# Kernel optimization log

Measured on AMD Instinct MI355X. Metric: run time of the kernel, lower is better.

Reference implementation:

```python
import jax, jax.numpy as jnp
import numpy as np

# hyper_params (mode='test')
PRE_NMS = 1000
POST_NMS = 300
IOU_TH = 0.7
VARIANCES = np.array([0.1, 0.1, 0.2, 0.2], dtype=np.float32)
FM = 64            # feature map height/width
ANCHOR_COUNT = 9   # 3 scales x 3 ratios


def _make_anchors():
    """Normalized [y1,x1,y2,x2] anchors on a FM x FM grid, 9 per cell."""
    scales = np.array([0.1, 0.2, 0.4], np.float32)
    ratios = np.array([0.5, 1.0, 2.0], np.float32)
    ws = (scales[:, None] * np.sqrt(ratios)[None, :]).reshape(-1)  # (9,)
    hs = (scales[:, None] / np.sqrt(ratios)[None, :]).reshape(-1)  # (9,)
    ctr = (np.arange(FM, dtype=np.float32) + 0.5) / FM
    cy, cx = np.meshgrid(ctr, ctr, indexing='ij')                  # (FM,FM)
    cy = cy[..., None]; cx = cx[..., None]                         # (FM,FM,1)
    anchors = np.stack([cy - 0.5 * hs, cx - 0.5 * ws,
                        cy + 0.5 * hs, cx + 0.5 * ws], axis=-1)    # (FM,FM,9,4)
    return jnp.asarray(anchors.reshape(-1, 4))                     # (36864,4)


def setup_inputs() -> dict:
    key = jax.random.key(0)
    k1, k2 = jax.random.split(key)
    B = 16
    rpn_bbox_deltas = jax.random.normal(k1, (B, FM, FM, ANCHOR_COUNT * 4), dtype=jnp.float32)
    rpn_labels = jax.random.uniform(k2, (B, FM, FM, ANCHOR_COUNT), dtype=jnp.float32)
    return {"rpn_bbox_deltas": rpn_bbox_deltas,
            "rpn_labels": rpn_labels,
            "anchors": _make_anchors()}


def _nms_single(boxes):
    """Greedy NMS on score-sorted boxes (N,4) -> (POST_NMS,4), zero-padded."""
    N = boxes.shape[0]
    y1, x1, y2, x2 = boxes[:, 0], boxes[:, 1], boxes[:, 2], boxes[:, 3]
    area = (y2 - y1) * (x2 - x1)                                   # (N,)
    iy1 = jnp.maximum(y1[:, None], y1[None, :])
    ix1 = jnp.maximum(x1[:, None], x1[None, :])
    iy2 = jnp.minimum(y2[:, None], y2[None, :])
    ix2 = jnp.minimum(x2[:, None], x2[None, :])
    inter = jnp.maximum(iy2 - iy1, 0.0) * jnp.maximum(ix2 - ix1, 0.0)
    iou = inter / jnp.maximum(area[:, None] + area[None, :] - inter, 1e-9)  # (N,N)
    idx = jnp.arange(N)

    def body(i, keep):
        # if box i survives, suppress later boxes with high overlap
        suppress = keep[i] & (iou[i] > IOU_TH) & (idx > i)
        return keep & ~suppress

    keep = jax.lax.fori_loop(0, N, body, jnp.ones((N,), dtype=bool))
    # stable sort: kept boxes first, original (score-descending) order preserved
    order = jnp.argsort(jnp.where(keep, 0, 1))[:POST_NMS]
    sel = boxes[order]
    valid = keep[order]
    # combined_non_max_suppression clips output boxes to [0,1] and zero-pads
    return jnp.where(valid[:, None], jnp.clip(sel, 0.0, 1.0), 0.0)


def reference(rpn_bbox_deltas, rpn_labels, anchors):
    B = rpn_bbox_deltas.shape[0]
    N = anchors.shape[0]
    deltas = rpn_bbox_deltas.reshape(B, N, 4) * jnp.asarray(VARIANCES)
    labels = rpn_labels.reshape(B, N)

    # decode deltas against anchors
    anc_h = anchors[:, 2] - anchors[:, 0]
    anc_w = anchors[:, 3] - anchors[:, 1]
    anc_cy = anchors[:, 0] + 0.5 * anc_h
    anc_cx = anchors[:, 1] + 0.5 * anc_w
    h = jnp.exp(deltas[..., 2]) * anc_h
    w = jnp.exp(deltas[..., 3]) * anc_w
    cy = deltas[..., 0] * anc_h + anc_cy
    cx = deltas[..., 1] * anc_w + anc_cx
    boxes = jnp.stack([cy - 0.5 * h, cx - 0.5 * w,
                       cy + 0.5 * h, cx + 0.5 * w], axis=-1)       # (B,N,4)

    # top-k by objectness score (descending, so NMS input is pre-sorted)
    _, pre_idx = jax.lax.top_k(labels, PRE_NMS)                    # (B,PRE_NMS)
    pre_boxes = jnp.take_along_axis(boxes, pre_idx[..., None], axis=1)  # (B,PRE_NMS,4)

    roi_bboxes = jax.vmap(_nms_single)(pre_boxes)                  # (B,POST_NMS,4)
    return jax.lax.stop_gradient(roi_bboxes)
```

## Files before the change

### kernel.cpp

```cpp
#include <hip/hip_runtime.h>
#include <stdint.h>

#pragma clang fp contract(off)

#define N_ANCH 36864
#define PRE_NMS 1000
#define POST_NMS 300
#define SEL_CAP 1024
#define NWAVE 16

#define SLICES 16
#define K1_NT 256
#define SLICE_KEYS 2304
#define KEYS_PT 9
#define SLICE_TOP 128
#define COMPACT_CAP 192
#define MERGE_CAP 2048

#define NCOPY 8
#define HSTR 257

#define M_WSTRIDE 1024
#define M_WORDS_PER_B 16384
#define WS_BOX_FLOATS_PER_B 5120

__device__ __forceinline__ uint32_t mono_key(float v) {
    uint32_t u = __float_as_uint(v);
    return (u & 0x80000000u) ? ~u : (u | 0x80000000u);
}

__device__ __forceinline__ float clip01(float x) {
    return fminf(fmaxf(x, 0.0f), 1.0f);
}

__device__ __forceinline__ uint64_t bcast64(uint64_t v, int srclane) {
    uint32_t lo = (uint32_t)v, hi = (uint32_t)(v >> 32);
    lo = __builtin_amdgcn_readlane(lo, srclane);
    hi = __builtin_amdgcn_readlane(hi, srclane);
    return ((uint64_t)hi << 32) | (uint64_t)lo;
}

__device__ __forceinline__ uint64_t sfl64(uint64_t v) {
    uint32_t lo = __builtin_amdgcn_readfirstlane((uint32_t)v);
    uint32_t hi = __builtin_amdgcn_readfirstlane((uint32_t)(v >> 32));
    return ((uint64_t)hi << 32) | (uint64_t)lo;
}

__device__ __forceinline__ uint64_t bfly_or64(uint64_t v) {
    v |= __shfl_xor(v, 32);
    v |= __shfl_xor(v, 16);
    v |= __shfl_xor(v, 8);
    v |= __shfl_xor(v, 4);
    v |= __shfl_xor(v, 2);
    v |= __shfl_xor(v, 1);
    return v;
}

__device__ __forceinline__ void scan256(const uint32_t* __restrict__ h, uint32_t K,
                                        uint32_t* shm, uint32_t& outBin, uint32_t& outKrem) {
    const int t    = threadIdx.x;
    const int lane = t & 63;
    const int wv   = t >> 6;
    const uint32_t q = h[t];
    uint32_t sfx = q, o;
    o = __shfl_down(sfx, 1);  if (lane < 63) sfx += o;
    o = __shfl_down(sfx, 2);  if (lane < 62) sfx += o;
    o = __shfl_down(sfx, 4);  if (lane < 60) sfx += o;
    o = __shfl_down(sfx, 8);  if (lane < 56) sfx += o;
    o = __shfl_down(sfx, 16); if (lane < 48) sfx += o;
    o = __shfl_down(sfx, 32); if (lane < 32) sfx += o;
    if (lane == 0) shm[wv] = sfx;
    __syncthreads();
    uint32_t wAbove = 0;
    for (int w2 = wv + 1; w2 < 4; ++w2) wAbove += shm[w2];
    const uint32_t above = wAbove + (sfx - q);
    if ((above < K) && (above + q >= K)) { shm[4] = (uint32_t)t; shm[5] = K - above; }
    __syncthreads();
    outBin  = shm[4];
    outKrem = shm[5];
}

__global__ __launch_bounds__(K1_NT) void k1s_slice_top(
    const float* __restrict__ labels,
    uint64_t* __restrict__ wsCand)
{
    const int s = blockIdx.x;
    const int b = blockIdx.y;
    const int t = threadIdx.x;
    const int lane = t & 63;

    __shared__ uint32_t hc[NCOPY * HSTR];
    __shared__ uint32_t red[256];
    __shared__ uint32_t shm[8];
    __shared__ uint64_t cand[COMPACT_CAP];
    __shared__ uint32_t scnt;

    const float* lab = labels + (size_t)b * N_ANCH + (size_t)s * SLICE_KEYS;
    uint32_t key[KEYS_PT];
#pragma unroll
    for (int r = 0; r < KEYS_PT; ++r)
        key[r] = mono_key(lab[r * K1_NT + t]);

    for (int i = t; i < NCOPY * HSTR; i += K1_NT) hc[i] = 0u;
    if (t == 0) scnt = 0u;
    __syncthreads();

    const int cbase = (lane & 7) * HSTR;
#pragma unroll
    for (int r = 0; r < KEYS_PT; ++r)
        atomicAdd(&hc[cbase + (key[r] >> 24)], 1u);
    __syncthreads();
    uint32_t sum = 0;
#pragma unroll
    for (int c = 0; c < NCOPY; ++c) sum += hc[c * HSTR + t];
    red[t] = sum;
    __syncthreads();
    uint32_t b0, krem;
    scan256(red, SLICE_TOP, shm, b0, krem);
    __syncthreads();

    red[t] = 0u;
    __syncthreads();
#pragma unroll
    for (int r = 0; r < KEYS_PT; ++r)
        if ((key[r] >> 24) == b0) atomicAdd(&red[(key[r] >> 16) & 0xFFu], 1u);
    __syncthreads();
    uint32_t b1, krem2;
    scan256(red, krem, shm, b1, krem2);
    const uint32_t thresh16 = (b0 << 8) | b1;

#pragma unroll
    for (int r = 0; r < KEYS_PT; ++r) {
        const uint32_t u = key[r];
        if ((u >> 16) >= thresh16) {
            const uint32_t gi = (uint32_t)(s * SLICE_KEYS + r * K1_NT + t);
            uint32_t pos = atomicAdd(&scnt, 1u);
            if (pos < COMPACT_CAP)
                cand[pos] = ((uint64_t)u << 32) | (uint64_t)(0xFFFFFFFFu - gi);
        }
    }
    __syncthreads();
    uint32_t c = scnt; if (c > COMPACT_CAP) c = COMPACT_CAP;
    if (t >= (int)c && t < COMPACT_CAP) cand[t] = 0ull;
    __syncthreads();

    if (t < COMPACT_CAP) {
        const uint64_t mine = cand[t];
        uint32_t rank = 0;
        for (int i = 0; i < COMPACT_CAP; i += 4)
            rank += (cand[i]     > mine) + (cand[i + 1] > mine)
                  + (cand[i + 2] > mine) + (cand[i + 3] > mine);
        if (t < (int)c && rank < SLICE_TOP)
            wsCand[((size_t)b * SLICES + s) * SLICE_TOP + rank] = mine;
    }
}

__global__ __launch_bounds__(K1_NT) void k1m_merge_decode(
    const float* __restrict__ deltas,
    const float* __restrict__ anchors,
    const uint64_t* __restrict__ wsCand,
    float* __restrict__ wsBox)
{
    const int chunk = blockIdx.x;
    const int b     = blockIdx.y;
    const int t     = threadIdx.x;

    __shared__ uint64_t keyA[MERGE_CAP];
    const uint64_t* c2 = wsCand + (size_t)b * MERGE_CAP;
    for (int i = t; i < MERGE_CAP; i += K1_NT) keyA[i] = c2[i];
    __syncthreads();

    if (t < SLICE_TOP) {
        const uint64_t mine = keyA[chunk * SLICE_TOP + t];
        uint32_t rank = 0;
#pragma unroll
        for (int r = 0; r < SLICES; ++r) {
            const uint64_t* a = &keyA[r * SLICE_TOP];
            uint32_t lo = 0;
#pragma unroll
            for (uint32_t s2 = 128; s2 > 0; s2 >>= 1)
                if (lo + s2 <= 128u && a[lo + s2 - 1] > mine) lo += s2;
            rank += lo;
        }
        if (rank < PRE_NMS) {
            uint32_t idx = 0xFFFFFFFFu - (uint32_t)(mine & 0xFFFFFFFFull);
            float4 d4 = *(const float4*)(deltas + ((size_t)b * N_ANCH + idx) * 4);
            float4 a4 = *(const float4*)(anchors + (size_t)idx * 4);
            float anc_h  = a4.z - a4.x;
            float anc_w  = a4.w - a4.y;
            float anc_cy = a4.x + 0.5f * anc_h;
            float anc_cx = a4.y + 0.5f * anc_w;
            float dy = d4.x * 0.1f, dx = d4.y * 0.1f;
            float dh = d4.z * 0.2f, dw = d4.w * 0.2f;
            float h  = expf(dh) * anc_h;
            float w  = expf(dw) * anc_w;
            float cy = dy * anc_h + anc_cy;
            float cx = dx * anc_w + anc_cx;
            float y1 = cy - 0.5f * h, x1 = cx - 0.5f * w;
            float y2 = cy + 0.5f * h, x2 = cx + 0.5f * w;
            float* wb = wsBox + (size_t)b * WS_BOX_FLOATS_PER_B;
            wb[rank]              = y1;
            wb[SEL_CAP + rank]    = x1;
            wb[2*SEL_CAP + rank]  = y2;
            wb[3*SEL_CAP + rank]  = x2;
            wb[4*SEL_CAP + rank]  = (y2 - y1) * (x2 - x1);
        }
    }
}

__global__ __launch_bounds__(1024) void k2_iou_matrix(
    const float* __restrict__ wsBox,
    uint64_t* __restrict__ wsM)
{
    const int gx   = blockIdx.x;
    const int b    = blockIdx.y;
    const int t    = threadIdx.x;
    const int lane = t & 63;
    const int wave = t >> 6;

    int cb, r0, r1;
    if (gx < 16) { cb = gx;     r0 = 0;   r1 = 64 * (cb + 1); if (r1 > 512) r1 = 512; }
    else         { cb = gx - 8; r0 = 512; r1 = 64 * (cb + 1); }
    if (r1 > PRE_NMS) r1 = PRE_NMS;

    __shared__ float s[5 * SEL_CAP];
    const float4* b4 = (const float4*)(wsBox + (size_t)b * WS_BOX_FLOATS_PER_B);
    float4* s4 = (float4*)s;
    for (int i = t; i < (5 * SEL_CAP) / 4; i += 1024) s4[i] = b4[i];
    __syncthreads();

    float* ly1 = s;
    float* lx1 = s + SEL_CAP;
    float* ly2 = s + 2 * SEL_CAP;
    float* lx2 = s + 3 * SEL_CAP;
    float* lar = s + 4 * SEL_CAP;

    const int j = cb * 64 + lane;
    const float y1j = ly1[j], x1j = lx1[j], y2j = ly2[j], x2j = lx2[j], aj = lar[j];

    uint64_t* Mb = wsM + (size_t)b * M_WORDS_PER_B + (size_t)cb * M_WSTRIDE;
    for (int i = r0 + wave; i < r1; i += NWAVE) {
        float iy1 = fmaxf(ly1[i], y1j);
        float ix1 = fmaxf(lx1[i], x1j);
        float iy2 = fminf(ly2[i], y2j);
        float ix2 = fminf(lx2[i], x2j);
        float ih = iy2 - iy1; if (ih < 0.f) ih = 0.f;
        float iw = ix2 - ix1; if (iw < 0.f) iw = 0.f;
        float inter = ih * iw;
        float denom = lar[i] + aj - inter;
        if (denom < 1e-9f) denom = 1e-9f;
        float iou = inter / denom;
        bool sup = (j > i) && (iou > 0.7f);
        uint64_t mask = __ballot(sup ? 1 : 0);
        if (lane == 0) Mb[i] = mask;
    }
}

__global__ __launch_bounds__(1024) void k3_reduce_out(
    const float* __restrict__ wsBox,
    const uint64_t* __restrict__ wsM,
    float* __restrict__ out)
{
    const int b    = blockIdx.x;
    const int t    = threadIdx.x;
    const int lane = t & 63;
    const int wave = t >> 6;

    __shared__ uint64_t remv[16];
    __shared__ uint64_t keepW[16];
    __shared__ uint32_t wordPref[16];

    const uint64_t* Mg = wsM + (size_t)b * M_WORDS_PER_B;

    if (t < 16) remv[t] = 0ull;

    uint64_t mDiag = 0ull, mSup = 0ull, selfC = 0ull;
    if (wave == 0) {
        mDiag = Mg[lane];
        mSup  = Mg[(size_t)1 * M_WSTRIDE + lane];
    }
    __syncthreads();

    for (int w = 0; w < 16; ++w) {
        if (wave == 0) {
            const uint64_t m  = mDiag;
            const uint64_t ms = mSup;
            if (w < 15) {
                mDiag = Mg[(size_t)(w + 1) * M_WSTRIDE + 64 * (w + 1) + lane];
                if (w < 14)
                    mSup = Mg[(size_t)(w + 2) * M_WSTRIDE + 64 * (w + 1) + lane];
            }
            const uint64_t valid = (w == 15) ? ((1ull << 40) - 1ull) : ~0ull;
            const bool laneValid = (w < 15) || (lane < 40);

            const uint64_t amS = sfl64(bfly_or64(laneValid ? m : 0ull));

            uint64_t cur = sfl64(remv[w] | selfC);

            const uint64_t Q        = amS & ~cur & valid;
            const uint64_t keptSure = valid & ~cur & ~Q;

            cur |= sfl64(bfly_or64(((keptSure >> lane) & 1ull) ? m : 0ull));

            uint64_t work = Q & ~cur;
            while (work) {
                const int bp = (int)__builtin_ctzll(work);
                cur |= bcast64(m, bp);
                work &= ~(1ull << bp);
                work &= ~cur;
            }

            const uint64_t keep = (~cur) & valid;
            if (lane == 0) keepW[w] = keep;
            if (w < 15)
                selfC = bfly_or64(((keep >> lane) & 1ull) ? ms : 0ull);
        } else if (w >= 1 && wave > w) {
            const uint64_t km = keepW[w - 1];
            uint64_t v = Mg[(size_t)wave * M_WSTRIDE + 64 * (w - 1) + lane];
            v = ((km >> lane) & 1ull) ? v : 0ull;
            v = bfly_or64(v);
            if (lane == 0) remv[wave] |= v;
        }
        __syncthreads();
    }

    if (t == 0) {
        uint32_t acc = 0u;
        for (int w = 0; w < 16; ++w) {
            wordPref[w] = acc;
            acc += (uint32_t)__popcll(keepW[w]);
        }
    }
    float* ob = out + (size_t)b * (POST_NMS * 4);
    for (int i = t; i < POST_NMS * 4; i += 1024) ob[i] = 0.0f;
    __syncthreads();

    if (t < PRE_NMS) {
        const int w = t >> 6, bpos = t & 63;
        uint64_t kw = keepW[w];
        if ((kw >> bpos) & 1ull) {
            uint32_t rank = wordPref[w] +
                            (uint32_t)__popcll(kw & ((1ull << bpos) - 1ull));
            if (rank < POST_NMS) {
                const float* wb = wsBox + (size_t)b * WS_BOX_FLOATS_PER_B;
                float* o = ob + (size_t)rank * 4;
                o[0] = clip01(wb[t]);
                o[1] = clip01(wb[SEL_CAP + t]);
                o[2] = clip01(wb[2*SEL_CAP + t]);
                o[3] = clip01(wb[3*SEL_CAP + t]);
            }
        }
    }
}

extern "C" void kernel_launch(void* const* d_in, const int* in_sizes, int n_in,
                              void* d_out, int out_size, void* d_ws, size_t ws_size,
                              hipStream_t stream) {
    const float* deltas  = (const float*)d_in[0];
    const float* labels  = (const float*)d_in[1];
    const float* anchors = (const float*)d_in[2];
    float* out = (float*)d_out;
    const int B = in_sizes[1] / N_ANCH;

    char* p = (char*)d_ws;
    uint64_t* wsCand = (uint64_t*)p;
    float*    wsBox  = (float*)(p + (size_t)B * MERGE_CAP * 8);
    uint64_t* wsM    = (uint64_t*)(p + (size_t)B * MERGE_CAP * 8
                                     + (size_t)B * WS_BOX_FLOATS_PER_B * 4);

    k1s_slice_top<<<dim3(SLICES, B), K1_NT, 0, stream>>>(labels, wsCand);
    k1m_merge_decode<<<dim3(SLICES, B), K1_NT, 0, stream>>>(deltas, anchors, wsCand, wsBox);
    k2_iou_matrix<<<dim3(24, B), 1024, 0, stream>>>(wsBox, wsM);
    k3_reduce_out<<<B, 1024, 0, stream>>>(wsBox, wsM, out);
}
```

Measured before the change: 110.8 us.

## Fuse IoU matrix and NMS reduce via last-block-done atomic counter

Merges the IoU bitmask kernel and the per-batch greedy reduction kernel into one launch. Each block increments a per-batch atomic counter after writing its mask words, and the last block to finish runs the NMS reduction and output write, reusing the boxes already held in shared memory. This removes one kernel launch and its gap, and the re-read of box data from global memory. In exchange it adds fences and an atomic per block, and the reduction is serialized onto whichever block arrives last.

```diff
diff --git a/kernel.cpp b/kernel.cpp
--- a/kernel.cpp
+++ b/kernel.cpp
@@ -23,6 +23,7 @@
 #define M_WSTRIDE 1024
 #define M_WORDS_PER_B 16384
 #define WS_BOX_FLOATS_PER_B 5120
+#define K2_BLOCKS_PER_B 24
 
 __device__ __forceinline__ uint32_t mono_key(float v) {
     uint32_t u = __float_as_uint(v);
@@ -82,12 +83,15 @@
 
 __global__ __launch_bounds__(K1_NT) void k1s_slice_top(
     const float* __restrict__ labels,
-    uint64_t* __restrict__ wsCand)
+    uint64_t* __restrict__ wsCand,
+    uint32_t* __restrict__ wsCnt)
 {
     const int s = blockIdx.x;
     const int b = blockIdx.y;
     const int t = threadIdx.x;
     const int lane = t & 63;
+
+    if (s == 0 && t == 0) wsCnt[b] = 0u;
 
     __shared__ uint32_t hc[NCOPY * HSTR];
     __shared__ uint32_t red[256];
@@ -208,9 +212,11 @@
     }
 }
 
-__global__ __launch_bounds__(1024) void k2_iou_matrix(
+__global__ __launch_bounds__(1024) void k2b_iou_nms(
     const float* __restrict__ wsBox,
-    uint64_t* __restrict__ wsM)
+    uint64_t* __restrict__ wsM,
+    uint32_t* __restrict__ wsCnt,
+    float* __restrict__ out)
 {
     const int gx   = blockIdx.x;
     const int b    = blockIdx.y;
@@ -254,17 +260,19 @@
         uint64_t mask = __ballot(sup ? 1 : 0);
         if (lane == 0) Mb[i] = mask;
     }
-}
-
-__global__ __launch_bounds__(1024) void k3_reduce_out(
-    const float* __restrict__ wsBox,
-    const uint64_t* __restrict__ wsM,
-    float* __restrict__ out)
-{
-    const int b    = blockIdx.x;
-    const int t    = threadIdx.x;
-    const int lane = t & 63;
-    const int wave = t >> 6;
+    __syncthreads();
+
+    __shared__ uint32_t isWinner;
+    if (t == 0) {
+        __threadfence();
+        uint32_t old = __hip_atomic_fetch_add(&wsCnt[b], 1u,
+                                              __ATOMIC_ACQ_REL,
+                                              __HIP_MEMORY_SCOPE_AGENT);
+        isWinner = (old == (uint32_t)(K2_BLOCKS_PER_B - 1));
+    }
+    __syncthreads();
+    if (!isWinner) return;
+    __threadfence();
 
     __shared__ uint64_t remv[16];
     __shared__ uint64_t keepW[16];
@@ -342,12 +350,11 @@
             uint32_t rank = wordPref[w] +
                             (uint32_t)__popcll(kw & ((1ull << bpos) - 1ull));
             if (rank < POST_NMS) {
-                const float* wb = wsBox + (size_t)b * WS_BOX_FLOATS_PER_B;
                 float* o = ob + (size_t)rank * 4;
-                o[0] = clip01(wb[t]);
-                o[1] = clip01(wb[SEL_CAP + t]);
-                o[2] = clip01(wb[2*SEL_CAP + t]);
-                o[3] = clip01(wb[3*SEL_CAP + t]);
+                o[0] = clip01(ly1[t]);
+                o[1] = clip01(lx1[t]);
+                o[2] = clip01(ly2[t]);
+                o[3] = clip01(lx2[t]);
             }
         }
     }
@@ -367,9 +374,11 @@
     float*    wsBox  = (float*)(p + (size_t)B * MERGE_CAP * 8);
     uint64_t* wsM    = (uint64_t*)(p + (size_t)B * MERGE_CAP * 8
                                      + (size_t)B * WS_BOX_FLOATS_PER_B * 4);
-
-    k1s_slice_top<<<dim3(SLICES, B), K1_NT, 0, stream>>>(labels, wsCand);
+    uint32_t* wsCnt  = (uint32_t*)(p + (size_t)B * MERGE_CAP * 8
+                                     + (size_t)B * WS_BOX_FLOATS_PER_B * 4
+                                     + (size_t)B * M_WORDS_PER_B * 8);
+
+    k1s_slice_top<<<dim3(SLICES, B), K1_NT, 0, stream>>>(labels, wsCand, wsCnt);
     k1m_merge_decode<<<dim3(SLICES, B), K1_NT, 0, stream>>>(deltas, anchors, wsCand, wsBox);
-    k2_iou_matrix<<<dim3(24, B), 1024, 0, stream>>>(wsBox, wsM);
-    k3_reduce_out<<<B, 1024, 0, stream>>>(wsBox, wsM, out);
-}
+    k2b_iou_nms<<<dim3(K2_BLOCKS_PER_B, B), 1024, 0, stream>>>(wsBox, wsM, wsCnt, out);
+}
```

New measurement: 142.9 us. 1.29x slower.

## Fuse merge-rank/decode into IoU kernel and prefetch reduce-stage mask words

Applied to the files above, without the earlier changes.

Drops the separate merge/decode kernel. Each of the 24 IoU blocks per image now ranks all 2048 candidates, decodes the top 1000 boxes straight into shared memory, and builds its IoU tile, so one launch and the global round-trip of the box workspace go away. Block 0 still writes box coordinates to global for the output stage, but no longer writes the area. The merge ranking and decode work is now repeated in every block, which adds redundant compute and extra anchor and delta gathers. The reduce kernel also prefetches the next mask word for the non-leader waves to hide global load latency.

```diff
diff --git a/kernel.cpp b/kernel.cpp
--- a/kernel.cpp
+++ b/kernel.cpp
@@ -155,23 +155,36 @@
     }
 }
 
-__global__ __launch_bounds__(K1_NT) void k1m_merge_decode(
+__global__ __launch_bounds__(1024) void k2f_rank_iou(
     const float* __restrict__ deltas,
     const float* __restrict__ anchors,
     const uint64_t* __restrict__ wsCand,
-    float* __restrict__ wsBox)
+    float* __restrict__ wsBox,
+    uint64_t* __restrict__ wsM)
 {
-    const int chunk = blockIdx.x;
-    const int b     = blockIdx.y;
-    const int t     = threadIdx.x;
+    const int gx   = blockIdx.x;
+    const int b    = blockIdx.y;
+    const int t    = threadIdx.x;
+    const int lane = t & 63;
+    const int wave = t >> 6;
 
     __shared__ uint64_t keyA[MERGE_CAP];
+    __shared__ float s[5 * SEL_CAP];
+
     const uint64_t* c2 = wsCand + (size_t)b * MERGE_CAP;
-    for (int i = t; i < MERGE_CAP; i += K1_NT) keyA[i] = c2[i];
-    __syncthreads();
-
-    if (t < SLICE_TOP) {
-        const uint64_t mine = keyA[chunk * SLICE_TOP + t];
+    for (int i = t; i < MERGE_CAP; i += 1024) keyA[i] = c2[i];
+    __syncthreads();
+
+    float* ly1 = s;
+    float* lx1 = s + SEL_CAP;
+    float* ly2 = s + 2 * SEL_CAP;
+    float* lx2 = s + 3 * SEL_CAP;
+    float* lar = s + 4 * SEL_CAP;
+
+#pragma unroll
+    for (int kk = 0; kk < 2; ++kk) {
+        const int ki = t + kk * 1024;
+        const uint64_t mine = keyA[ki];
         uint32_t rank = 0;
 #pragma unroll
         for (int r = 0; r < SLICES; ++r) {
@@ -198,42 +211,26 @@
             float cx = dx * anc_w + anc_cx;
             float y1 = cy - 0.5f * h, x1 = cx - 0.5f * w;
             float y2 = cy + 0.5f * h, x2 = cx + 0.5f * w;
-            float* wb = wsBox + (size_t)b * WS_BOX_FLOATS_PER_B;
-            wb[rank]              = y1;
-            wb[SEL_CAP + rank]    = x1;
-            wb[2*SEL_CAP + rank]  = y2;
-            wb[3*SEL_CAP + rank]  = x2;
-            wb[4*SEL_CAP + rank]  = (y2 - y1) * (x2 - x1);
-        }
-    }
-}
-
-__global__ __launch_bounds__(1024) void k2_iou_matrix(
-    const float* __restrict__ wsBox,
-    uint64_t* __restrict__ wsM)
-{
-    const int gx   = blockIdx.x;
-    const int b    = blockIdx.y;
-    const int t    = threadIdx.x;
-    const int lane = t & 63;
-    const int wave = t >> 6;
+            ly1[rank] = y1;
+            lx1[rank] = x1;
+            ly2[rank] = y2;
+            lx2[rank] = x2;
+            lar[rank] = (y2 - y1) * (x2 - x1);
+            if (gx == 0) {
+                float* wb = wsBox + (size_t)b * WS_BOX_FLOATS_PER_B;
+                wb[rank]             = y1;
+                wb[SEL_CAP + rank]   = x1;
+                wb[2*SEL_CAP + rank] = y2;
+                wb[3*SEL_CAP + rank] = x2;
+            }
+        }
+    }
+    __syncthreads();
 
     int cb, r0, r1;
     if (gx < 16) { cb = gx;     r0 = 0;   r1 = 64 * (cb + 1); if (r1 > 512) r1 = 512; }
     else         { cb = gx - 8; r0 = 512; r1 = 64 * (cb + 1); }
     if (r1 > PRE_NMS) r1 = PRE_NMS;
-
-    __shared__ float s[5 * SEL_CAP];
-    const float4* b4 = (const float4*)(wsBox + (size_t)b * WS_BOX_FLOATS_PER_B);
-    float4* s4 = (float4*)s;
-    for (int i = t; i < (5 * SEL_CAP) / 4; i += 1024) s4[i] = b4[i];
-    __syncthreads();
-
-    float* ly1 = s;
-    float* lx1 = s + SEL_CAP;
-    float* ly2 = s + 2 * SEL_CAP;
-    float* lx2 = s + 3 * SEL_CAP;
-    float* lar = s + 4 * SEL_CAP;
 
     const int j = cb * 64 + lane;
     const float y1j = ly1[j], x1j = lx1[j], y2j = ly2[j], x2j = lx2[j], aj = lar[j];
@@ -274,10 +271,12 @@
 
     if (t < 16) remv[t] = 0ull;
 
-    uint64_t mDiag = 0ull, mSup = 0ull, selfC = 0ull;
+    uint64_t mDiag = 0ull, mSup = 0ull, selfC = 0ull, mRed = 0ull;
     if (wave == 0) {
         mDiag = Mg[lane];
         mSup  = Mg[(size_t)1 * M_WSTRIDE + lane];
+    } else if (wave >= 2) {
+        mRed  = Mg[(size_t)wave * M_WSTRIDE + lane];
     }
     __syncthreads();
 
@@ -315,8 +314,10 @@
             if (w < 15)
                 selfC = bfly_or64(((keep >> lane) & 1ull) ? ms : 0ull);
         } else if (w >= 1 && wave > w) {
+            uint64_t v = mRed;
+            if (wave > w + 1)
+                mRed = Mg[(size_t)wave * M_WSTRIDE + 64 * w + lane];
             const uint64_t km = keepW[w - 1];
-            uint64_t v = Mg[(size_t)wave * M_WSTRIDE + 64 * (w - 1) + lane];
             v = ((km >> lane) & 1ull) ? v : 0ull;
             v = bfly_or64(v);
             if (lane == 0) remv[wave] |= v;
@@ -369,7 +370,6 @@
                                      + (size_t)B * WS_BOX_FLOATS_PER_B * 4);
 
     k1s_slice_top<<<dim3(SLICES, B), K1_NT, 0, stream>>>(labels, wsCand);
-    k1m_merge_decode<<<dim3(SLICES, B), K1_NT, 0, stream>>>(deltas, anchors, wsCand, wsBox);
-    k2_iou_matrix<<<dim3(24, B), 1024, 0, stream>>>(wsBox, wsM);
+    k2f_rank_iou<<<dim3(24, B), 1024, 0, stream>>>(deltas, anchors, wsCand, wsBox, wsM);
     k3_reduce_out<<<B, 1024, 0, stream>>>(wsBox, wsM, out);
 }
```

Measured after the change: 119.0 us. 7.3% more time.
